# Performance work log

Hardware: AMD Instinct MI355X
Metric: run time of the kernel (lower is better)

Reference implementation:

```python
import jax, jax.numpy as jnp
import numpy as np

H = 8          # query heads
KVH = 4        # key/value heads
D = 256        # head_dim
HID = 2304     # hidden_size
B = 1
S = 4096
SW = 2048      # sliding window
THETA = 10000.0
SCALE = 256 ** -0.5          # query_pre_attn_scalar ** -0.5
SOFTCAP = 50.0
NEG = -1e9


def setup_inputs() -> dict:
    key = jax.random.key(0)
    ks = jax.random.split(key, 6)
    hidden_states = jax.random.normal(ks[0], (B, S, HID), jnp.float32)
    Wq = jax.random.normal(ks[1], (H * D, HID), jnp.float32) * 0.02
    Wk = jax.random.normal(ks[2], (KVH * D, HID), jnp.float32) * 0.02
    Wv = jax.random.normal(ks[3], (KVH * D, HID), jnp.float32) * 0.02
    Wo = jax.random.normal(ks[4], (HID, H * D), jnp.float32) * 0.02
    # causal + sliding-window additive mask: allowed iff 0 <= i-j < SW
    i = jnp.arange(S)[:, None]
    j = jnp.arange(S)[None, :]
    ok = (i >= j) & ((i - j) < SW)
    attention_mask = jnp.where(ok, 0.0, NEG).astype(jnp.float32)[None, None]
    position_ids = jnp.arange(S, dtype=jnp.int32)[None, :]
    return {"hidden_states": hidden_states, "attention_mask": attention_mask,
            "Wq": Wq, "Wk": Wk, "Wv": Wv, "Wo": Wo, "position_ids": position_ids}


def _rope(q, k, position_ids):
    # cos/sin: [B, 1, S, D]
    pos = position_ids.astype(jnp.float32)                      # [B, S]
    inv_freq = 1.0 / (THETA ** (jnp.arange(0, D, 2, dtype=jnp.float32) / D))
    freqs = pos[:, :, None] * inv_freq[None, None, :]           # [B, S, D/2]
    emb = jnp.concatenate([freqs, freqs], axis=-1)              # [B, S, D]
    cos = jnp.cos(emb)[:, None]
    sin = jnp.sin(emb)[:, None]
    rot = lambda x: jnp.concatenate([-x[..., D // 2:], x[..., :D // 2]], axis=-1)
    return q * cos + rot(q) * sin, k * cos + rot(k) * sin


def reference(hidden_states, attention_mask, Wq, Wk, Wv, Wo, position_ids):
    b, s, _ = hidden_states.shape
    q = (hidden_states @ Wq.T).reshape(b, s, H, D).transpose(0, 2, 1, 3)    # [B,H,S,D]
    k = (hidden_states @ Wk.T).reshape(b, s, KVH, D).transpose(0, 2, 1, 3)  # [B,KVH,S,D]
    v = (hidden_states @ Wv.T).reshape(b, s, KVH, D).transpose(0, 2, 1, 3)
    q, k = _rope(q, k, position_ids)
    rep = H // KVH
    k = jnp.repeat(k, rep, axis=1)
    v = jnp.repeat(v, rep, axis=1)
    scores = jnp.einsum('bhqd,bhkd->bhqk', q * SCALE, k)
    scores = jnp.tanh(scores / SOFTCAP) * SOFTCAP + attention_mask
    probs = jax.nn.softmax(scores.astype(jnp.float32), axis=-1).astype(q.dtype)
    out = jnp.einsum('bhqk,bhkd->bhqd', probs, v)
    out = out.transpose(0, 2, 1, 3).reshape(b, s, H * D)
    return out @ Wo.T
```

## Files before the change

### kernel.cpp

```cpp
#include <hip/hip_runtime.h>
#include <hip/hip_bf16.h>
#include <math.h>

#define S 4096
#define HQ 8
#define NKVH 4
#define D 256
#define HID 2304
#define SW 2048
#define QDIM 2048
#define KVDIM 1024
#define QKVDIM 4096
#define SCALE 0.0625f
#define SOFTCAP 50.0f

typedef __attribute__((ext_vector_type(4))) float f32x4;
typedef __attribute__((ext_vector_type(8))) short short8;

__device__ __forceinline__ float bf2f(unsigned v) { return __uint_as_float(v << 16); }
__device__ __forceinline__ unsigned f2bf(float f) {
    unsigned u = __float_as_uint(f);
    return (u + 0x7fffu + ((u >> 16) & 1u)) >> 16;
}

__device__ __forceinline__ void store_c(float* p, float v) { *p = v; }
__device__ __forceinline__ void store_c(unsigned short* p, float v) { *p = (unsigned short)f2bf(v); }

__device__ __forceinline__ void glls16(const void* g, void* l) {
    __builtin_amdgcn_global_load_lds(
        (const __attribute__((address_space(1))) unsigned int*)g,
        (__attribute__((address_space(3))) unsigned int*)l, 16, 0, 0);
}

__global__ __launch_bounds__(256) void cvt_bf16(const float* __restrict__ in,
                                                unsigned short* __restrict__ out)
{
    int i = blockIdx.x * 256 + threadIdx.x;
    float4 v = ((const float4*)in)[i];
    uint2 o;
    o.x = f2bf(v.x) | (f2bf(v.y) << 16);
    o.y = f2bf(v.z) | (f2bf(v.w) << 16);
    ((uint2*)out)[i] = o;
}

template <typename TC>
__global__ __launch_bounds__(256) void bf16_gemm_bt(const unsigned short* __restrict__ A,
                                                    const unsigned short* __restrict__ B,
                                                    TC* __restrict__ C,
                                                    int M, int N, int K)
{
    __shared__ unsigned short As[2][16 * 512];
    __shared__ unsigned short Bs[2][16 * 512];
    const int t = threadIdx.x;

    const int nbx = gridDim.x;
    const int nwg = nbx * gridDim.y;
    int flat = blockIdx.y * nbx + blockIdx.x;
    const int q8 = nwg >> 3, r8 = nwg & 7;
    const int xcd = flat & 7, orig = flat >> 3;
    const int wg = (xcd < r8 ? xcd * (q8 + 1) : r8 * (q8 + 1) + (xcd - r8) * q8) + orig;
    const int band = wg / (8 * nbx);
    const int rem  = wg - band * 8 * nbx;
    const int m0 = (band * 8 + (rem & 7)) * 128;
    const int n0 = (rem >> 3) * 128;

    const int w = t >> 6, lid = t & 63, n16 = lid & 15, quad = lid >> 4;
    const int wm = (w >> 1) * 64, wn = (w & 1) * 64;

    f32x4 acc[4][4] = {};

    auto stage = [&](int buf, int k0) {
        #pragma unroll
        for (int it = 0; it < 4; ++it) {
            int f  = it * 4 + w;
            int fm = f >> 1, fk = f & 1;
            const size_t goff = (size_t)(fm * 16 + n16) * K + k0 + fk * 32 + quad * 8;
            glls16(A + (size_t)m0 * K + goff, &As[buf][f * 512]);
            glls16(B + (size_t)n0 * K + goff, &Bs[buf][f * 512]);
        }
    };

    const int nk = K / 64;
    stage(0, 0);
    int cur = 0;
    for (int kk = 0; kk < nk; ++kk) {
        asm volatile("s_waitcnt vmcnt(0)" ::: "memory");
        __syncthreads();
        if (kk + 1 < nk) stage(cur ^ 1, (kk + 1) * 64);
        #pragma unroll
        for (int ks = 0; ks < 2; ++ks) {
            short8 af[4], bfr[4];
            #pragma unroll
            for (int x = 0; x < 4; ++x) {
                af[x]  = *(const short8*)(&As[cur][(((wm >> 4) + x) * 2 + ks) * 512 + lid * 8]);
                bfr[x] = *(const short8*)(&Bs[cur][(((wn >> 4) + x) * 2 + ks) * 512 + lid * 8]);
            }
            __builtin_amdgcn_s_setprio(1);
            #pragma unroll
            for (int i = 0; i < 4; ++i)
                #pragma unroll
                for (int j = 0; j < 4; ++j)
                    acc[i][j] = __builtin_amdgcn_mfma_f32_16x16x32_bf16(af[i], bfr[j], acc[i][j], 0, 0, 0);
            __builtin_amdgcn_s_setprio(0);
        }
        cur ^= 1;
    }

    #pragma unroll
    for (int i = 0; i < 4; ++i) {
        #pragma unroll
        for (int j = 0; j < 4; ++j) {
            int rbase = m0 + wm + i * 16 + quad * 4;
            int col   = n0 + wn + j * 16 + n16;
            #pragma unroll
            for (int rg = 0; rg < 4; ++rg)
                store_c(C + (size_t)(rbase + rg) * N + col, acc[i][j][rg]);
        }
    }
}

__global__ __launch_bounds__(512, 2) void bf16_gemm_8ph(const unsigned short* __restrict__ A,
                                                        const unsigned short* __restrict__ B,
                                                        unsigned short* __restrict__ C,
                                                        int M, int N, int K)
{
    __shared__ unsigned short As[2][32 * 512];
    __shared__ unsigned short Bs[2][32 * 512];
    const int t = threadIdx.x;
    const int w = t >> 6, lid = t & 63, n16 = lid & 15, quad = lid >> 4;

    const int flat = blockIdx.x;
    const int wg = (flat & 7) * 32 + (flat >> 3);
    const int m0 = (wg >> 4) * 256, n0 = (wg & 15) * 256;

    const int wmf = (w >> 2) * 8;
    const int wnf = (w & 3) * 4;
    const int fnw = (w >> 1) * 4 + (w & 1);

    f32x4 acc[8][4] = {};

    auto stageA = [&](int buf, int k0, int fm) {
        glls16(A + (size_t)(m0 + fm * 16 + n16) * K + k0 + quad * 8,
               &As[buf][(fm * 2 + 0) * 512]);
        glls16(A + (size_t)(m0 + fm * 16 + n16) * K + k0 + 32 + quad * 8,
               &As[buf][(fm * 2 + 1) * 512]);
    };
    auto stageB = [&](int buf, int k0, int fn) {
        glls16(B + (size_t)(n0 + fn * 16 + n16) * K + k0 + quad * 8,
               &Bs[buf][(fn * 2 + 0) * 512]);
        glls16(B + (size_t)(n0 + fn * 16 + n16) * K + k0 + 32 + quad * 8,
               &Bs[buf][(fn * 2 + 1) * 512]);
    };
    auto sAm0 = [&](int buf, int k0){ stageA(buf, k0, (w & 3) + (w >> 2) * 8); };
    auto sAm1 = [&](int buf, int k0){ stageA(buf, k0, 4 + (w & 3) + (w >> 2) * 8); };
    auto sBn0 = [&](int buf, int k0){ stageB(buf, k0, fnw); };
    auto sBn1 = [&](int buf, int k0){ stageB(buf, k0, fnw + 2); };

#define GPHASE(mh, nh, buf, STAGE, WAITSTR)                                          \
    {                                                                                \
        short8 afr[4][2], bfr[2][2];                                                 \
        _Pragma("unroll") for (int i = 0; i < 4; ++i)                                \
            _Pragma("unroll") for (int ks = 0; ks < 2; ++ks)                         \
                afr[i][ks] = *(const short8*)(&As[buf][((wmf + (mh)*4 + i)*2 + ks)*512 + lid*8]); \
        _Pragma("unroll") for (int j = 0; j < 2; ++j)                                \
            _Pragma("unroll") for (int ks = 0; ks < 2; ++ks)                         \
                bfr[j][ks] = *(const short8*)(&Bs[buf][((wnf + (nh)*2 + j)*2 + ks)*512 + lid*8]); \
        STAGE;                                                                       \
        __builtin_amdgcn_s_barrier();                                                \
        asm volatile("s_waitcnt lgkmcnt(0)" ::: "memory");                           \
        __builtin_amdgcn_sched_barrier(0);                                           \
        __builtin_amdgcn_s_setprio(1);                                               \
        _Pragma("unroll") for (int i = 0; i < 4; ++i)                                \
            _Pragma("unroll") for (int j = 0; j < 2; ++j)                            \
                _Pragma("unroll") for (int ks = 0; ks < 2; ++ks)                     \
                    acc[(mh)*4 + i][(nh)*2 + j] = __builtin_amdgcn_mfma_f32_16x16x32_bf16( \
                        afr[i][ks], bfr[j][ks], acc[(mh)*4 + i][(nh)*2 + j], 0, 0, 0); \
        __builtin_amdgcn_s_setprio(0);                                               \
        asm volatile(WAITSTR ::: "memory");                                          \
        __builtin_amdgcn_s_barrier();                                                \
    }

    const int nk = K / 64;
    const int niter = nk / 2;

    sAm0(0, 0); sBn0(0, 0); sAm1(0, 0); sBn1(0, 0);
    sAm0(1, 64); sBn0(1, 64);
    asm volatile("s_waitcnt vmcnt(4)" ::: "memory");
    __builtin_amdgcn_s_barrier();

    for (int I = 0; I < niter - 1; ++I) {
        const int kc = I * 128;
        GPHASE(0, 0, 0, sAm1(1, kc + 64);,  "")
        GPHASE(0, 1, 0, sBn1(1, kc + 64);,  "")
        GPHASE(1, 0, 0, sAm0(0, kc + 128);, "")
        GPHASE(1, 1, 0, sBn0(0, kc + 128);, "s_waitcnt vmcnt(4)")
        GPHASE(0, 0, 1, sAm1(0, kc + 128);, "")
        GPHASE(0, 1, 1, sBn1(0, kc + 128);, "")
        GPHASE(1, 0, 1, sAm0(1, kc + 192);, "")
        GPHASE(1, 1, 1, sBn0(1, kc + 192);, "s_waitcnt vmcnt(4)")
    }
    {
        const int kc = (niter - 1) * 128;
        GPHASE(0, 0, 0, sAm1(1, kc + 64);, "")
        GPHASE(0, 1, 0, sBn1(1, kc + 64);, "")
        GPHASE(1, 0, 0, {};,               "")
        GPHASE(1, 1, 0, {};,               "s_waitcnt vmcnt(0)")
        GPHASE(0, 0, 1, {};,               "")
        GPHASE(0, 1, 1, {};,               "")
        GPHASE(1, 0, 1, {};,               "")
        GPHASE(1, 1, 1, {};,               "")
    }
#undef GPHASE

    #pragma unroll
    for (int mi = 0; mi < 8; ++mi) {
        #pragma unroll
        for (int nj = 0; nj < 4; ++nj) {
            int rbase = m0 + (w >> 2) * 128 + mi * 16 + quad * 4;
            int col   = n0 + (w & 3) * 64 + nj * 16 + n16;
            #pragma unroll
            for (int rg = 0; rg < 4; ++rg)
                store_c(C + (size_t)(rbase + rg) * N + col, acc[mi][nj][rg]);
        }
    }
}

__global__ __launch_bounds__(256) void rope_kernel(const unsigned short* __restrict__ QKV,
                                                   unsigned short* __restrict__ Qb,
                                                   unsigned short* __restrict__ Kb,
                                                   const int* __restrict__ pos_ids)
{
    int id   = blockIdx.x * 256 + threadIdx.x;
    int d    = id & 127;
    int rest = id >> 7;
    int hh   = rest % 12;
    int i    = rest / 12;
    float pos = (float)pos_ids[i];
    float inv = __expf((float)d * (-9.210340371976184f / 128.0f));
    float ang = pos * inv;
    float sn, cs;
    sincosf(ang, &sn, &cs);
    if (hh < HQ) {
        const unsigned short* p = QKV + (size_t)i * QKVDIM + hh * D + d;
        float x0 = bf2f(p[0]), x1 = bf2f(p[128]);
        unsigned short* q = Qb + (size_t)i * QDIM + hh * D + d;
        q[0]   = (unsigned short)f2bf((x0 * cs - x1 * sn) * SCALE);
        q[128] = (unsigned short)f2bf((x1 * cs + x0 * sn) * SCALE);
    } else {
        const unsigned short* p = QKV + (size_t)i * QKVDIM + QDIM + (hh - HQ) * D + d;
        float x0 = bf2f(p[0]), x1 = bf2f(p[128]);
        unsigned short* k = Kb + (size_t)i * KVDIM + (hh - HQ) * D + d;
        k[0]   = (unsigned short)f2bf(x0 * cs - x1 * sn);
        k[128] = (unsigned short)f2bf(x1 * cs + x0 * sn);
    }
}

__global__ __launch_bounds__(256) void transpose_v(const unsigned short* __restrict__ QKV,
                                                   unsigned short* __restrict__ Vt)
{
    __shared__ float tile[64][65];
    const int s0 = blockIdx.x * 64, d0 = blockIdx.y * 64;
    const int t = threadIdx.x;
    #pragma unroll
    for (int it = 0; it < 4; ++it) {
        int flat = it * 256 + t;
        int r  = flat >> 4;
        int c4 = (flat & 15) * 4;
        uint2 v = *(const uint2*)(QKV + (size_t)(s0 + r) * QKVDIM + (QDIM + KVDIM) + d0 + c4);
        tile[r][c4 + 0] = bf2f(v.x & 0xffffu); tile[r][c4 + 1] = bf2f(v.x >> 16);
        tile[r][c4 + 2] = bf2f(v.y & 0xffffu); tile[r][c4 + 3] = bf2f(v.y >> 16);
    }
    __syncthreads();
    #pragma unroll
    for (int it = 0; it < 4; ++it) {
        int flat = it * 256 + t;
        int dr  = flat >> 4;
        int sc4 = (flat & 15) * 4;
        uint2 o;
        o.x = f2bf(tile[sc4 + 0][dr]) | (f2bf(tile[sc4 + 1][dr]) << 16);
        o.y = f2bf(tile[sc4 + 2][dr]) | (f2bf(tile[sc4 + 3][dr]) << 16);
        *(uint2*)(Vt + (size_t)(d0 + dr) * S + s0 + sc4) = o;
    }
}

__global__ __launch_bounds__(256, 2) void attn_kernel(const unsigned short* __restrict__ Qb,
                                                      const unsigned short* __restrict__ Kb,
                                                      const unsigned short* __restrict__ Vt,
                                                      unsigned short* __restrict__ O)
{
    __shared__ unsigned short Ks[2][32 * 256];
    __shared__ unsigned short Vs[2][256 * 32];
    __shared__ unsigned short Ps[4 * 512];
    const int t = threadIdx.x;
    const int bid = blockIdx.x;
    const int b2 = bid & 255;
    const int h = b2 & 7, kvh = h >> 1;
    const int u = b2 >> 3;
    const int g = (bid < 256) ? u : 63 - u;
    const int i0 = g * 64;
    const int w = t >> 6, lid = t & 63, n16 = lid & 15, quad = lid >> 4;
    const int qbase = i0 + w * 16;
    unsigned short* Pw = Ps + w * 512;

    auto stage = [&](int buf, int j0) {
        #pragma unroll
        for (int it = 0; it < 4; ++it) {
            int f = it * 4 + w;
            int nt = f >> 3, ks = f & 7;
            glls16(Kb + (size_t)(j0 + nt * 16 + n16) * KVDIM + kvh * D + ks * 32 + quad * 8,
                   &Ks[buf][f * 512]);
        }
        #pragma unroll
        for (int it = 0; it < 4; ++it) {
            int f = it * 4 + w;
            glls16(Vt + (size_t)(kvh * D + f * 16 + n16) * S + j0 + quad * 8,
                   &Vs[buf][f * 512]);
        }
    };

    short8 qf[8];
    #pragma unroll
    for (int ks = 0; ks < 8; ++ks)
        qf[ks] = *(const short8*)(Qb + (size_t)(qbase + n16) * QDIM + h * D + ks * 32 + quad * 8);

    float lacc[4] = {0.f, 0.f, 0.f, 0.f};
    f32x4 Oacc[16] = {};

    const int jt_min = (i0 >= SW) ? ((i0 - (SW - 1)) >> 5) : 0;
    const int jt_max = (i0 + 63) >> 5;

    stage(0, jt_min * 32);
    int cur = 0;

    for (int jt = jt_min; jt <= jt_max; ++jt) {
        const int j0 = jt * 32;
        asm volatile("s_waitcnt vmcnt(0)" ::: "memory");
        __syncthreads();
        if (jt < jt_max) stage(cur ^ 1, (jt + 1) * 32);

        f32x4 sc[2] = {};
        __builtin_amdgcn_s_setprio(1);
        #pragma unroll
        for (int ks = 0; ks < 8; ++ks) {
            #pragma unroll
            for (int nt = 0; nt < 2; ++nt) {
                short8 kf = *(const short8*)(&Ks[cur][(nt * 8 + ks) * 512 + lid * 8]);
                sc[nt] = __builtin_amdgcn_mfma_f32_16x16x32_bf16(qf[ks], kf, sc[nt], 0, 0, 0);
            }
        }
        __builtin_amdgcn_s_setprio(0);

        #pragma unroll
        for (int nt = 0; nt < 2; ++nt) {
            int j = j0 + nt * 16 + n16;
            #pragma unroll
            for (int rg = 0; rg < 4; ++rg) {
                int iq = qbase + quad * 4 + rg;
                float e = __expf(sc[nt][rg] * (2.0f / SOFTCAP));
                float p = __expf(-100.0f * __builtin_amdgcn_rcpf(e + 1.0f));
                bool ok = (j <= iq) && (iq - j < SW);
                p = ok ? p : 0.0f;
                lacc[rg] += p;
                Pw[(quad * 4 + rg + 16 * (nt * 2 + (n16 >> 3))) * 8 + (n16 & 7)]
                    = (unsigned short)f2bf(p);
            }
        }

        asm volatile("s_waitcnt lgkmcnt(0)" ::: "memory");

        short8 pf = *(const short8*)(Pw + lid * 8);
        __builtin_amdgcn_s_setprio(1);
        #pragma unroll
        for (int dt = 0; dt < 16; ++dt) {
            short8 vf = *(const short8*)(&Vs[cur][dt * 512 + lid * 8]);
            Oacc[dt] = __builtin_amdgcn_mfma_f32_16x16x32_bf16(pf, vf, Oacc[dt], 0, 0, 0);
        }
        __builtin_amdgcn_s_setprio(0);
        cur ^= 1;
    }

    float linv[4];
    #pragma unroll
    for (int rg = 0; rg < 4; ++rg) {
        float rs = lacc[rg];
        rs += __shfl_xor(rs, 1); rs += __shfl_xor(rs, 2);
        rs += __shfl_xor(rs, 4); rs += __shfl_xor(rs, 8);
        linv[rg] = 1.0f / rs;
    }
    #pragma unroll
    for (int dt = 0; dt < 16; ++dt) {
        int col = h * D + dt * 16 + n16;
        #pragma unroll
        for (int rg = 0; rg < 4; ++rg) {
            int row = qbase + quad * 4 + rg;
            O[(size_t)row * QDIM + col] = (unsigned short)f2bf(Oacc[dt][rg] * linv[rg]);
        }
    }
}

extern "C" void kernel_launch(void* const* d_in, const int* in_sizes, int n_in,
                              void* d_out, int out_size, void* d_ws, size_t ws_size,
                              hipStream_t stream) {
    const float* hidden = (const float*)d_in[0];
    const float* Wq = (const float*)d_in[2];
    const float* Wk = (const float*)d_in[3];
    const float* Wv = (const float*)d_in[4];
    const float* Wo = (const float*)d_in[5];
    const int* pos = (const int*)d_in[6];
    float* out = (float*)d_out;

    char* ws = (char*)d_ws;
    unsigned short* Hb   = (unsigned short*)(ws);
    unsigned short* Qb   = (unsigned short*)(ws);
    unsigned short* Wqkv = (unsigned short*)(ws + (size_t)(18 << 20));
    unsigned short* QKVf = (unsigned short*)(ws + (size_t)(37 << 20));
    unsigned short* Oa   = (unsigned short*)(ws + (size_t)(37 << 20));
    unsigned short* Kb   = (unsigned short*)(ws + (size_t)(69 << 20));
    unsigned short* Vt   = (unsigned short*)(ws + (size_t)(77 << 20));

    cvt_bf16<<<(S * HID) / 1024, 256, 0, stream>>>(hidden, Hb);
    cvt_bf16<<<(QDIM * HID) / 1024, 256, 0, stream>>>(Wq, Wqkv);
    cvt_bf16<<<(KVDIM * HID) / 1024, 256, 0, stream>>>(Wk, Wqkv + (size_t)QDIM * HID);
    cvt_bf16<<<(KVDIM * HID) / 1024, 256, 0, stream>>>(Wv, Wqkv + (size_t)(QDIM + KVDIM) * HID);

    bf16_gemm_8ph<<<256, 512, 0, stream>>>(Hb, Wqkv, QKVf, S, QKVDIM, HID);

    rope_kernel<<<(S * 12 * 128) / 256, 256, 0, stream>>>(QKVf, Qb, Kb, pos);
    transpose_v<<<dim3(S / 64, KVDIM / 64), 256, 0, stream>>>(QKVf, Vt);

    attn_kernel<<<512, 256, 0, stream>>>(Qb, Kb, Vt, Oa);

    cvt_bf16<<<(HID * QDIM) / 1024, 256, 0, stream>>>(Wo, Wqkv);
    bf16_gemm_bt<float><<<dim3(HID / 128, S / 128), 256, 0, stream>>>(Oa, Wqkv, out, S, HID, QDIM);
}
```

Baseline: 568.7 us.

## Split KV range of long attention rows across two blocks and add combine kernel

Query tiles from row 1024 onward have their key range split into two halves, each handled by its own block. Each half writes unnormalized bf16 partial outputs and row sums, and a new combine kernel adds them and normalizes. Short rows still run unsplit. The launch grows from 512 to 896 blocks to improve load balance and occupancy across CUs, at the cost of an extra kernel, extra global traffic for the partials, and some bf16 rounding in the unnormalized partials. Merging the halves without max rescaling relies on the softcap keeping scores bounded.

Measured after the change: 572.5 us. No clear change (+0.7%).

```diff
diff --git a/kernel.cpp b/kernel.cpp
--- a/kernel.cpp
+++ b/kernel.cpp
@@ -286,21 +286,45 @@
 __global__ __launch_bounds__(256, 2) void attn_kernel(const unsigned short* __restrict__ Qb,
                                                       const unsigned short* __restrict__ Kb,
                                                       const unsigned short* __restrict__ Vt,
-                                                      unsigned short* __restrict__ O)
+                                                      unsigned short* __restrict__ O,
+                                                      unsigned short* __restrict__ Op0,
+                                                      unsigned short* __restrict__ Op1,
+                                                      float* __restrict__ Lp0,
+                                                      float* __restrict__ Lp1)
 {
     __shared__ unsigned short Ks[2][32 * 256];
     __shared__ unsigned short Vs[2][256 * 32];
     __shared__ unsigned short Ps[4 * 512];
     const int t = threadIdx.x;
     const int bid = blockIdx.x;
-    const int b2 = bid & 255;
-    const int h = b2 & 7, kvh = h >> 1;
-    const int u = b2 >> 3;
-    const int g = (bid < 256) ? u : 63 - u;
+
+    int h, g, half;
+    bool split;
+    if (bid < 768) {
+        split = true;
+        h = bid & 7;
+        int rest = bid >> 3;
+        half = rest & 1;
+        g = 63 - (rest >> 1);
+    } else {
+        split = false;
+        h = bid & 7;
+        half = 0;
+        g = 15 - ((bid - 768) >> 3);
+    }
+    const int kvh = h >> 1;
     const int i0 = g * 64;
     const int w = t >> 6, lid = t & 63, n16 = lid & 15, quad = lid >> 4;
     const int qbase = i0 + w * 16;
     unsigned short* Pw = Ps + w * 512;
+
+    const int jlo = (i0 >= SW) ? ((i0 - (SW - 1)) >> 5) : 0;
+    const int jhi = (i0 + 63) >> 5;
+    int jt0 = jlo, jt1 = jhi;
+    if (split) {
+        int mid = (jlo + jhi + 1) >> 1;
+        if (half == 0) jt1 = mid - 1; else jt0 = mid;
+    }
 
     auto stage = [&](int buf, int j0) {
         #pragma unroll
@@ -326,17 +350,14 @@
     float lacc[4] = {0.f, 0.f, 0.f, 0.f};
     f32x4 Oacc[16] = {};
 
-    const int jt_min = (i0 >= SW) ? ((i0 - (SW - 1)) >> 5) : 0;
-    const int jt_max = (i0 + 63) >> 5;
-
-    stage(0, jt_min * 32);
+    stage(0, jt0 * 32);
     int cur = 0;
 
-    for (int jt = jt_min; jt <= jt_max; ++jt) {
+    for (int jt = jt0; jt <= jt1; ++jt) {
         const int j0 = jt * 32;
         asm volatile("s_waitcnt vmcnt(0)" ::: "memory");
         __syncthreads();
-        if (jt < jt_max) stage(cur ^ 1, (jt + 1) * 32);
+        if (jt < jt1) stage(cur ^ 1, (jt + 1) * 32);
 
         f32x4 sc[2] = {};
         __builtin_amdgcn_s_setprio(1);
@@ -379,23 +400,67 @@
         cur ^= 1;
     }
 
-    float linv[4];
+    float rsum[4];
     #pragma unroll
     for (int rg = 0; rg < 4; ++rg) {
         float rs = lacc[rg];
         rs += __shfl_xor(rs, 1); rs += __shfl_xor(rs, 2);
         rs += __shfl_xor(rs, 4); rs += __shfl_xor(rs, 8);
-        linv[rg] = 1.0f / rs;
-    }
-    #pragma unroll
-    for (int dt = 0; dt < 16; ++dt) {
-        int col = h * D + dt * 16 + n16;
-        #pragma unroll
-        for (int rg = 0; rg < 4; ++rg) {
-            int row = qbase + quad * 4 + rg;
-            O[(size_t)row * QDIM + col] = (unsigned short)f2bf(Oacc[dt][rg] * linv[rg]);
-        }
-    }
+        rsum[rg] = rs;
+    }
+
+    if (!split) {
+        #pragma unroll
+        for (int dt = 0; dt < 16; ++dt) {
+            int col = h * D + dt * 16 + n16;
+            #pragma unroll
+            for (int rg = 0; rg < 4; ++rg) {
+                int row = qbase + quad * 4 + rg;
+                O[(size_t)row * QDIM + col] = (unsigned short)f2bf(Oacc[dt][rg] / rsum[rg]);
+            }
+        }
+    } else {
+        unsigned short* Op = half ? Op1 : Op0;
+        float* Lp = half ? Lp1 : Lp0;
+        if (n16 == 0) {
+            #pragma unroll
+            for (int rg = 0; rg < 4; ++rg)
+                Lp[(size_t)(qbase - 1024 + quad * 4 + rg) * 8 + h] = rsum[rg];
+        }
+        #pragma unroll
+        for (int dt = 0; dt < 16; ++dt) {
+            int col = h * D + dt * 16 + n16;
+            #pragma unroll
+            for (int rg = 0; rg < 4; ++rg) {
+                int prow = qbase - 1024 + quad * 4 + rg;
+                Op[(size_t)prow * QDIM + col] = (unsigned short)f2bf(Oacc[dt][rg]);
+            }
+        }
+    }
+}
+
+__global__ __launch_bounds__(256) void attn_combine(const unsigned short* __restrict__ Op0,
+                                                    const unsigned short* __restrict__ Op1,
+                                                    const float* __restrict__ Lp0,
+                                                    const float* __restrict__ Lp1,
+                                                    unsigned short* __restrict__ O)
+{
+    int tid = blockIdx.x * 256 + threadIdx.x;
+    int row = tid >> 8;
+    int c8  = (tid & 255) * 8;
+    int h   = c8 >> 8;
+    float rinv = 1.0f / (Lp0[(size_t)row * 8 + h] + Lp1[(size_t)row * 8 + h]);
+    uint4 a = *(const uint4*)(Op0 + (size_t)row * QDIM + c8);
+    uint4 b = *(const uint4*)(Op1 + (size_t)row * QDIM + c8);
+    auto comb = [&](unsigned ua, unsigned ub) {
+        float x0 = (bf2f(ua & 0xffffu) + bf2f(ub & 0xffffu)) * rinv;
+        float x1 = (bf2f(ua >> 16) + bf2f(ub >> 16)) * rinv;
+        return f2bf(x0) | (f2bf(x1) << 16);
+    };
+    uint4 o;
+    o.x = comb(a.x, b.x); o.y = comb(a.y, b.y);
+    o.z = comb(a.z, b.z); o.w = comb(a.w, b.w);
+    *(uint4*)(O + (size_t)(row + 1024) * QDIM + c8) = o;
 }
 
 extern "C" void kernel_launch(void* const* d_in, const int* in_sizes, int n_in,
@@ -415,6 +480,10 @@
     unsigned short* Wqkv = (unsigned short*)(ws + (size_t)(18 << 20));
     unsigned short* QKVf = (unsigned short*)(ws + (size_t)(37 << 20));
     unsigned short* Oa   = (unsigned short*)(ws + (size_t)(37 << 20));
+    unsigned short* Op0  = (unsigned short*)(ws + (size_t)(18 << 20));
+    float*          Lp0  = (float*)(ws + (size_t)(18 << 20) + (size_t)(13 << 20));
+    unsigned short* Op1  = (unsigned short*)(ws + (size_t)(53 << 20));
+    float*          Lp1  = (float*)(ws + (size_t)(53 << 20) + (size_t)(13 << 20));
     unsigned short* Kb   = (unsigned short*)(ws + (size_t)(69 << 20));
     unsigned short* Vt   = (unsigned short*)(ws + (size_t)(77 << 20));
 
@@ -428,7 +497,8 @@
     rope_kernel<<<(S * 12 * 128) / 256, 256, 0, stream>>>(QKVf, Qb, Kb, pos);
     transpose_v<<<dim3(S / 64, KVDIM / 64), 256, 0, stream>>>(QKVf, Vt);
 
-    attn_kernel<<<512, 256, 0, stream>>>(Qb, Kb, Vt, Oa);
+    attn_kernel<<<896, 256, 0, stream>>>(Qb, Kb, Vt, Oa, Op0, Op1, Lp0, Lp1);
+    attn_combine<<<3072, 256, 0, stream>>>(Op0, Op1, Lp0, Lp1, Oa);
 
     cvt_bf16<<<(HID * QDIM) / 1024, 256, 0, stream>>>(Wo, Wqkv);
     bf16_gemm_bt<float><<<dim3(HID / 128, S / 128), 256, 0, stream>>>(Oa, Wqkv, out, S, HID, QDIM);
```

## Switch attention K/V staging to register prefetch with 64-key tiles

Applied to the files above, without the earlier changes.

Replaces the double-buffered direct global-to-LDS loads with a register-staged prefetch. The next K/V tile is loaded into registers while the current one is computed, then written to a single LDS buffer after a barrier. It also doubles the key tile from 32 to 64, halving the number of loop iterations and barriers. The cost is many more VGPRs for the prefetch buffers (16 uint4 per thread), which may hurt occupancy under launch_bounds(256,2). It also adds a second barrier per iteration and more masked work at the diagonal and window edges.

After: 800.8 us. +40.8%, slower.

```diff
diff --git a/kernel.cpp b/kernel.cpp
--- a/kernel.cpp
+++ b/kernel.cpp
@@ -288,9 +288,9 @@
                                                       const unsigned short* __restrict__ Vt,
                                                       unsigned short* __restrict__ O)
 {
-    __shared__ unsigned short Ks[2][32 * 256];
-    __shared__ unsigned short Vs[2][256 * 32];
-    __shared__ unsigned short Ps[4 * 512];
+    __shared__ unsigned short Ks[32 * 512];
+    __shared__ unsigned short Vs[32 * 512];
+    __shared__ unsigned short Ps[4 * 1024];
     const int t = threadIdx.x;
     const int bid = blockIdx.x;
     const int b2 = bid & 255;
@@ -300,21 +300,34 @@
     const int i0 = g * 64;
     const int w = t >> 6, lid = t & 63, n16 = lid & 15, quad = lid >> 4;
     const int qbase = i0 + w * 16;
-    unsigned short* Pw = Ps + w * 512;
-
-    auto stage = [&](int buf, int j0) {
-        #pragma unroll
-        for (int it = 0; it < 4; ++it) {
+    unsigned short* Pw = Ps + w * 1024;
+
+    uint4 kr[8], vr[8];
+
+    auto issue = [&](int j0) {
+        #pragma unroll
+        for (int it = 0; it < 8; ++it) {
             int f = it * 4 + w;
             int nt = f >> 3, ks = f & 7;
-            glls16(Kb + (size_t)(j0 + nt * 16 + n16) * KVDIM + kvh * D + ks * 32 + quad * 8,
-                   &Ks[buf][f * 512]);
-        }
-        #pragma unroll
-        for (int it = 0; it < 4; ++it) {
+            kr[it] = *(const uint4*)(Kb + (size_t)(j0 + nt * 16 + n16) * KVDIM + kvh * D + ks * 32 + quad * 8);
+        }
+        #pragma unroll
+        for (int it = 0; it < 8; ++it) {
             int f = it * 4 + w;
-            glls16(Vt + (size_t)(kvh * D + f * 16 + n16) * S + j0 + quad * 8,
-                   &Vs[buf][f * 512]);
+            int dt = f >> 1, ks2 = f & 1;
+            vr[it] = *(const uint4*)(Vt + (size_t)(kvh * D + dt * 16 + n16) * S + j0 + ks2 * 32 + quad * 8);
+        }
+    };
+    auto commit = [&]() {
+        #pragma unroll
+        for (int it = 0; it < 8; ++it) {
+            int f = it * 4 + w;
+            *(uint4*)(&Ks[f * 512 + lid * 8]) = kr[it];
+        }
+        #pragma unroll
+        for (int it = 0; it < 8; ++it) {
+            int f = it * 4 + w;
+            *(uint4*)(&Vs[f * 512 + lid * 8]) = vr[it];
         }
     };
 
@@ -326,32 +339,32 @@
     float lacc[4] = {0.f, 0.f, 0.f, 0.f};
     f32x4 Oacc[16] = {};
 
-    const int jt_min = (i0 >= SW) ? ((i0 - (SW - 1)) >> 5) : 0;
-    const int jt_max = (i0 + 63) >> 5;
-
-    stage(0, jt_min * 32);
-    int cur = 0;
+    const int jt_min = (i0 >= SW) ? ((i0 - (SW - 1)) >> 6) : 0;
+    const int jt_max = (i0 + 63) >> 6;
+
+    issue(jt_min * 64);
 
     for (int jt = jt_min; jt <= jt_max; ++jt) {
-        const int j0 = jt * 32;
+        const int j0 = jt * 64;
         asm volatile("s_waitcnt vmcnt(0)" ::: "memory");
+        commit();
         __syncthreads();
-        if (jt < jt_max) stage(cur ^ 1, (jt + 1) * 32);
-
-        f32x4 sc[2] = {};
+        if (jt < jt_max) issue((jt + 1) * 64);
+
+        f32x4 sc[4] = {};
         __builtin_amdgcn_s_setprio(1);
         #pragma unroll
         for (int ks = 0; ks < 8; ++ks) {
             #pragma unroll
-            for (int nt = 0; nt < 2; ++nt) {
-                short8 kf = *(const short8*)(&Ks[cur][(nt * 8 + ks) * 512 + lid * 8]);
+            for (int nt = 0; nt < 4; ++nt) {
+                short8 kf = *(const short8*)(&Ks[(nt * 8 + ks) * 512 + lid * 8]);
                 sc[nt] = __builtin_amdgcn_mfma_f32_16x16x32_bf16(qf[ks], kf, sc[nt], 0, 0, 0);
             }
         }
         __builtin_amdgcn_s_setprio(0);
 
         #pragma unroll
-        for (int nt = 0; nt < 2; ++nt) {
+        for (int nt = 0; nt < 4; ++nt) {
             int j = j0 + nt * 16 + n16;
             #pragma unroll
             for (int rg = 0; rg < 4; ++rg) {
@@ -361,22 +374,26 @@
                 bool ok = (j <= iq) && (iq - j < SW);
                 p = ok ? p : 0.0f;
                 lacc[rg] += p;
-                Pw[(quad * 4 + rg + 16 * (nt * 2 + (n16 >> 3))) * 8 + (n16 & 7)]
+                Pw[(nt >> 1) * 512 + (quad * 4 + rg + 16 * ((nt & 1) * 2 + (n16 >> 3))) * 8 + (n16 & 7)]
                     = (unsigned short)f2bf(p);
             }
         }
 
         asm volatile("s_waitcnt lgkmcnt(0)" ::: "memory");
 
-        short8 pf = *(const short8*)(Pw + lid * 8);
+        short8 pf0 = *(const short8*)(Pw + lid * 8);
+        short8 pf1 = *(const short8*)(Pw + 512 + lid * 8);
         __builtin_amdgcn_s_setprio(1);
         #pragma unroll
         for (int dt = 0; dt < 16; ++dt) {
-            short8 vf = *(const short8*)(&Vs[cur][dt * 512 + lid * 8]);
-            Oacc[dt] = __builtin_amdgcn_mfma_f32_16x16x32_bf16(pf, vf, Oacc[dt], 0, 0, 0);
+            short8 vf0 = *(const short8*)(&Vs[(dt * 2 + 0) * 512 + lid * 8]);
+            Oacc[dt] = __builtin_amdgcn_mfma_f32_16x16x32_bf16(pf0, vf0, Oacc[dt], 0, 0, 0);
+            short8 vf1 = *(const short8*)(&Vs[(dt * 2 + 1) * 512 + lid * 8]);
+            Oacc[dt] = __builtin_amdgcn_mfma_f32_16x16x32_bf16(pf1, vf1, Oacc[dt], 0, 0, 0);
         }
         __builtin_amdgcn_s_setprio(0);
-        cur ^= 1;
+
+        __syncthreads();
     }
 
     float linv[4];
```
